# Kernel optimization log

Measured on AMD Instinct MI355X. Metric: run time of the kernel, lower is better.

Reference implementation:

```python
import jax, jax.numpy as jnp
import numpy as np

B, N, DIM = 4, 4096, 512
H, DH = 8, 64
F = 256          # nb_features = min(256, int(log(4096)*32)) = 256
CS = 128         # chunk_size = min(128, n)


def setup_inputs() -> dict:
    key = jax.random.key(0)
    k1, k2, k3, k4 = jax.random.split(key, 4)
    x = jax.random.normal(k1, (B, N, DIM), jnp.float32)
    # scale linear weights like default init so activations stay well-conditioned
    w_qkv = jax.random.normal(k2, (3 * H * DH, DIM), jnp.float32) / jnp.sqrt(DIM)
    w_out = jax.random.normal(k3, (DIM, H * DH), jnp.float32) / jnp.sqrt(H * DH)
    b_out = jnp.zeros((DIM,), jnp.float32)
    # torch.qr(randn(F, DH)) -> reduced Q of shape (F, DH), orthonormal columns
    proj = jnp.linalg.qr(jax.random.normal(k4, (F, DH), jnp.float32))[0]
    return {"x": x, "w_qkv": w_qkv, "w_out": w_out, "b_out": b_out, "proj": proj}


def _kernel_fn(t, proj):
    # exp(x @ proj^T - rowmax), stabilized over the feature axis (as in source)
    tp = jnp.einsum('...d,fd->...f', t, proj)
    return jnp.exp(tp - jnp.max(tp, axis=-1, keepdims=True))


def reference(x, w_qkv, w_out, b_out, proj):
    b, n, _ = x.shape
    scale = DH ** -0.5
    c = n // CS  # number of independent local chunks

    qkv = x @ w_qkv.T                                   # [b, n, 3*h*d]
    q, k, v = jnp.split(qkv, 3, axis=-1)

    def to_chunks(t):  # [b, n, h*d] -> [b, h, c, cs, d]
        return t.reshape(b, n, H, DH).transpose(0, 2, 1, 3).reshape(b, H, c, CS, DH)

    q = to_chunks(q) * scale
    k = to_chunks(k)
    v = to_chunks(v)

    q_prime = _kernel_fn(q, proj)                       # [b, h, c, cs, f]
    k_prime = _kernel_fn(k, proj)                       # [b, h, c, cs, f]

    k_sum = k_prime.sum(axis=3)                         # [b, h, c, f]
    D = jnp.einsum('bhcsf,bhcf->bhcs', q_prime, k_sum)
    D_inv = 1.0 / (D + 0.0001)

    context = jnp.einsum('bhcsf,bhcsd->bhcfd', k_prime, v)     # [b, h, c, f, d]
    out = jnp.einsum('bhcsf,bhcfd->bhcsd', q_prime, context)   # [b, h, c, cs, d]
    out = out * D_inv[..., None]

    out = out.reshape(b, H, n, DH).transpose(0, 2, 1, 3).reshape(b, n, H * DH)
    return out @ w_out.T + b_out                        # dropout p=0 -> identity
```

## Files before the change

kernel.cpp:

```cpp
#include <hip/hip_runtime.h>

#define B_ 4
#define N_ 4096
#define DIM_ 512
#define H_ 8
#define DH_ 64
#define F_ 256
#define CS_ 128
#define M_ (B_*N_)
#define NCHUNK_ 1024

typedef __attribute__((ext_vector_type(8))) short bf16x8;
typedef __attribute__((ext_vector_type(4))) float f32x4;

__device__ __forceinline__ unsigned short f2bf(float x){
  unsigned int u = __float_as_uint(x);
  u += 0x7fffu + ((u >> 16) & 1u);
  return (unsigned short)(u >> 16);
}
__device__ __forceinline__ float bf2f(unsigned short s){
  return __uint_as_float(((unsigned int)s) << 16);
}
__device__ __forceinline__ unsigned pack2(float a, float b){
  return (unsigned)f2bf(a) | ((unsigned)f2bf(b) << 16);
}
__device__ __forceinline__ void gl2lds16(const unsigned short* g, unsigned short* l) {
  __builtin_amdgcn_global_load_lds((const __attribute__((address_space(1))) unsigned int*)g,
                                   (__attribute__((address_space(3))) unsigned int*)l,
                                   16, 0, 0);
}

__global__ __launch_bounds__(256)
void split_kernel(const float* __restrict__ src, unsigned short* __restrict__ hi,
                  unsigned short* __restrict__ lo, int n4)
{
  int idx = blockIdx.x * 256 + threadIdx.x;
  if (idx >= n4) return;
  float4 v = ((const float4*)src)[idx];
  unsigned short h0 = f2bf(v.x), h1 = f2bf(v.y), h2 = f2bf(v.z), h3 = f2bf(v.w);
  unsigned short e0 = f2bf(v.x - bf2f(h0)), e1 = f2bf(v.y - bf2f(h1));
  unsigned short e2 = f2bf(v.z - bf2f(h2)), e3 = f2bf(v.w - bf2f(h3));
  uint2 hv, lv;
  hv.x = (unsigned)h0 | ((unsigned)h1 << 16); hv.y = (unsigned)h2 | ((unsigned)h3 << 16);
  lv.x = (unsigned)e0 | ((unsigned)e1 << 16); lv.y = (unsigned)e2 | ((unsigned)e3 << 16);
  ((uint2*)hi)[idx] = hv;
  ((uint2*)lo)[idx] = lv;
}

__global__ __launch_bounds__(256)
void prep_proj(const float* __restrict__ proj, unsigned short* __restrict__ pq,
               unsigned short* __restrict__ pk)
{
  int idx = blockIdx.x * 256 + threadIdx.x;
  if (idx >= 4096) return;
  float4 v = ((const float4*)proj)[idx];
  uint2 k, q;
  k.x = pack2(v.x, v.y);           k.y = pack2(v.z, v.w);
  q.x = pack2(v.x*0.125f, v.y*0.125f); q.y = pack2(v.z*0.125f, v.w*0.125f);
  ((uint2*)pk)[idx] = k;
  ((uint2*)pq)[idx] = q;
}

template<int SPLIT, int OUT>
__global__ __launch_bounds__(256, 2)
void mfma_gemm_nt(const unsigned short* __restrict__ Ahi, const unsigned short* __restrict__ Alo,
                  const unsigned short* __restrict__ Bhi, const unsigned short* __restrict__ Blo,
                  void* __restrict__ Cm, const float* __restrict__ bias, int K, int ldc,
                  unsigned short* __restrict__ vth, unsigned short* __restrict__ vtl)
{
  __shared__ __align__(16) unsigned short sAhi[4096];
  __shared__ __align__(16) unsigned short sBhi[4096];
  __shared__ __align__(16) unsigned short sAlo[4096];
  __shared__ __align__(16) unsigned short sBlo[4096];
  const int tid = threadIdx.x, lane = tid & 63, wave = tid >> 6;
  const int bm = blockIdx.y * 128, bn = blockIdx.x * 128;
  const int srow0 = wave * 32 + (lane >> 2);
  const int srow1 = srow0 + 16;
  const int slot = lane & 3;
  const int g0 = slot ^ ((srow0 >> 1) & 3);
  const int g1 = slot ^ ((srow1 >> 1) & 3);
  const size_t aOff0 = (size_t)(bm + srow0) * K + g0 * 8;
  const size_t aOff1 = (size_t)(bm + srow1) * K + g1 * 8;
  const size_t bOff0 = (size_t)(bn + srow0) * K + g0 * 8;
  const size_t bOff1 = (size_t)(bn + srow1) * K + g1 * 8;
  const int l0 = wave * 1024, l1 = wave * 1024 + 512;
  const int fr = lane & 15, quad = lane >> 4;
  const int wr = (wave >> 1) * 64, wc = (wave & 1) * 64;
  int offA[4], offB[4];
#pragma unroll
  for (int i = 0; i < 4; ++i) {
    int ra = wr + i * 16 + fr;  offA[i] = ra * 32 + (quad ^ ((ra >> 1) & 3)) * 8;
    int rb = wc + i * 16 + fr;  offB[i] = rb * 32 + (quad ^ ((rb >> 1) & 3)) * 8;
  }
  f32x4 acc[4][4];
#pragma unroll
  for (int i = 0; i < 4; ++i)
#pragma unroll
    for (int j = 0; j < 4; ++j) acc[i][j] = {0.f, 0.f, 0.f, 0.f};

  for (int k0 = 0; k0 < K; k0 += 32) {
    gl2lds16(Ahi + aOff0 + k0, &sAhi[l0]);
    gl2lds16(Ahi + aOff1 + k0, &sAhi[l1]);
    gl2lds16(Bhi + bOff0 + k0, &sBhi[l0]);
    gl2lds16(Bhi + bOff1 + k0, &sBhi[l1]);
    if (SPLIT) {
      gl2lds16(Alo + aOff0 + k0, &sAlo[l0]);
      gl2lds16(Alo + aOff1 + k0, &sAlo[l1]);
      gl2lds16(Blo + bOff0 + k0, &sBlo[l0]);
      gl2lds16(Blo + bOff1 + k0, &sBlo[l1]);
    }
    __syncthreads();
    bf16x8 ah[4], bh[4], al[4], bl[4];
#pragma unroll
    for (int i = 0; i < 4; ++i) {
      ah[i] = *(const bf16x8*)&sAhi[offA[i]];
      bh[i] = *(const bf16x8*)&sBhi[offB[i]];
      if (SPLIT) {
        al[i] = *(const bf16x8*)&sAlo[offA[i]];
        bl[i] = *(const bf16x8*)&sBlo[offB[i]];
      }
    }
#pragma unroll
    for (int i = 0; i < 4; ++i)
#pragma unroll
      for (int j = 0; j < 4; ++j) {
        acc[i][j] = __builtin_amdgcn_mfma_f32_16x16x32_bf16(ah[i], bh[j], acc[i][j], 0, 0, 0);
        if (SPLIT) {
          acc[i][j] = __builtin_amdgcn_mfma_f32_16x16x32_bf16(ah[i], bl[j], acc[i][j], 0, 0, 0);
          acc[i][j] = __builtin_amdgcn_mfma_f32_16x16x32_bf16(al[i], bh[j], acc[i][j], 0, 0, 0);
        }
      }
    __syncthreads();
  }
#pragma unroll
  for (int j = 0; j < 4; ++j) {
    int col = bn + wc + j * 16 + fr;
    float bv = (OUT == 0 && bias) ? bias[col] : 0.f;
#pragma unroll
    for (int i = 0; i < 4; ++i) {
      int row0 = bm + wr + i * 16 + quad * 4;
      if (OUT == 0) {
        float* cp = (float*)Cm + (size_t)row0 * ldc + col;
#pragma unroll
        for (int r = 0; r < 4; ++r) cp[(size_t)r * ldc] = acc[i][j][r] + bv;
      } else if (OUT == 1) {
        unsigned short* cp = (unsigned short*)Cm + (size_t)row0 * ldc + col;
#pragma unroll
        for (int r = 0; r < 4; ++r) cp[(size_t)r * ldc] = f2bf(acc[i][j][r]);
      } else {
        int hh = col >> 6, d = col & 63;
        int bb = row0 >> 12, cc2 = (row0 >> 7) & 31, s = row0 & 127;
        int ck = bb * 256 + hh * 32 + cc2;
        size_t ad = (size_t)ck * 8192 + d * 128 + (((s >> 3) ^ (d & 15)) << 3) + (s & 7);
        float v0 = acc[i][j][0], v1 = acc[i][j][1], v2 = acc[i][j][2], v3 = acc[i][j][3];
        unsigned short h0 = f2bf(v0), h1 = f2bf(v1), h2 = f2bf(v2), h3 = f2bf(v3);
        uint2 hv, lv;
        hv.x = (unsigned)h0 | ((unsigned)h1 << 16);
        hv.y = (unsigned)h2 | ((unsigned)h3 << 16);
        lv.x = pack2(v0 - bf2f(h0), v1 - bf2f(h1));
        lv.y = pack2(v2 - bf2f(h2), v3 - bf2f(h3));
        *(uint2*)(vth + ad) = hv;
        *(uint2*)(vtl + ad) = lv;
      }
    }
  }
}

__global__ __launch_bounds__(256, 2)
void feat_kernel(const unsigned short* __restrict__ qkv_bf,
                 const unsigned short* __restrict__ projq,
                 const unsigned short* __restrict__ projk,
                 unsigned short* __restrict__ qp_g, unsigned short* __restrict__ kpT_g,
                 float* __restrict__ ksum_g)
{
  __shared__ __align__(16) unsigned short IN[8192];
  __shared__ __align__(16) unsigned short BOUNCE[16384];
  __shared__ float KSP[4][256];
  const int tid = threadIdx.x, lane = tid & 63, wave = tid >> 6;
  const int fr = lane & 15, quad = lane >> 4;
  const int chunk = blockIdx.x, p = blockIdx.y;
  const int b = chunk >> 8, h = (chunk >> 5) & 7, cc = chunk & 31;
  const int mbase = b * N_ + cc * CS_;
  const int colbase = p * DIM_ + h * DH_;

#pragma unroll
  for (int j = 0; j < 8; ++j) {
    int idx = tid + j * 256;
    int s = idx >> 4, d0 = (idx & 15) * 4;
    uint2 v = *(const uint2*)(qkv_bf + (size_t)(mbase + s) * 1024 + colbase + d0);
    *(uint2*)(IN + s * 64 + (((d0 >> 3) ^ (s & 7)) << 3) + (d0 & 7)) = v;
  }
  __syncthreads();

  if (p == 0) {
    f32x4 acc[16][2];
#pragma unroll
    for (int mt = 0; mt < 16; ++mt) { acc[mt][0] = {0,0,0,0}; acc[mt][1] = {0,0,0,0}; }
#pragma unroll
    for (int ks = 0; ks < 2; ++ks) {
      bf16x8 bfr[2];
#pragma unroll
      for (int nt = 0; nt < 2; ++nt) {
        int s = wave * 32 + nt * 16 + fr;
        bfr[nt] = *(const bf16x8*)(IN + s * 64 + (((ks * 4 + quad) ^ (s & 7)) << 3));
      }
#pragma unroll
      for (int mt = 0; mt < 16; ++mt) {
        bf16x8 af = *(const bf16x8*)(projq + (size_t)(mt * 16 + fr) * 64 + ks * 32 + quad * 8);
        acc[mt][0] = __builtin_amdgcn_mfma_f32_16x16x32_bf16(af, bfr[0], acc[mt][0], 0, 0, 0);
        acc[mt][1] = __builtin_amdgcn_mfma_f32_16x16x32_bf16(af, bfr[1], acc[mt][1], 0, 0, 0);
      }
    }
#pragma unroll
    for (int nt = 0; nt < 2; ++nt) {
      float m = -1e30f;
#pragma unroll
      for (int mt = 0; mt < 16; ++mt)
#pragma unroll
        for (int r = 0; r < 4; ++r) m = fmaxf(m, acc[mt][nt][r]);
      m = fmaxf(m, __shfl_xor(m, 16, 64));
      m = fmaxf(m, __shfl_xor(m, 32, 64));
#pragma unroll
      for (int mt = 0; mt < 16; ++mt)
#pragma unroll
        for (int r = 0; r < 4; ++r) acc[mt][nt][r] = __expf(acc[mt][nt][r] - m);
    }
    unsigned short* dst = qp_g + (size_t)chunk * 32768;
#pragma unroll
    for (int hf = 0; hf < 2; ++hf) {
      if ((wave >> 1) == hf) {
#pragma unroll
        for (int nt = 0; nt < 2; ++nt) {
          int sl = (wave & 1) * 32 + nt * 16 + fr;
#pragma unroll
          for (int mt = 0; mt < 16; ++mt) {
            int g = mt * 2 + (quad >> 1);
            uint2 w;
            w.x = pack2(acc[mt][nt][0], acc[mt][nt][1]);
            w.y = pack2(acc[mt][nt][2], acc[mt][nt][3]);
            *(uint2*)(BOUNCE + sl * 256 + ((g ^ fr) << 3) + (quad & 1) * 4) = w;
          }
        }
      }
      __syncthreads();
#pragma unroll
      for (int j2 = 0; j2 < 8; ++j2) {
        int idx = j2 * 256 + tid;
        *(float4*)(dst + (size_t)hf * 16384 + idx * 8) = *(const float4*)(BOUNCE + idx * 8);
      }
      __syncthreads();
    }
  } else {
    f32x4 acc[2][16];
#pragma unroll
    for (int nt = 0; nt < 16; ++nt) { acc[0][nt] = {0,0,0,0}; acc[1][nt] = {0,0,0,0}; }
#pragma unroll
    for (int ks = 0; ks < 2; ++ks) {
      bf16x8 a[2];
#pragma unroll
      for (int mt = 0; mt < 2; ++mt) {
        int s = wave * 32 + mt * 16 + fr;
        a[mt] = *(const bf16x8*)(IN + s * 64 + (((ks * 4 + quad) ^ (s & 7)) << 3));
      }
#pragma unroll
      for (int nt = 0; nt < 16; ++nt) {
        bf16x8 bf = *(const bf16x8*)(projk + (size_t)(nt * 16 + fr) * 64 + ks * 32 + quad * 8);
        acc[0][nt] = __builtin_amdgcn_mfma_f32_16x16x32_bf16(a[0], bf, acc[0][nt], 0, 0, 0);
        acc[1][nt] = __builtin_amdgcn_mfma_f32_16x16x32_bf16(a[1], bf, acc[1][nt], 0, 0, 0);
      }
    }
#pragma unroll
    for (int mt = 0; mt < 2; ++mt)
#pragma unroll
      for (int r = 0; r < 4; ++r) {
        float m = acc[mt][0][r];
#pragma unroll
        for (int nt = 1; nt < 16; ++nt) m = fmaxf(m, acc[mt][nt][r]);
        m = fmaxf(m, __shfl_xor(m, 1, 16));
        m = fmaxf(m, __shfl_xor(m, 2, 16));
        m = fmaxf(m, __shfl_xor(m, 4, 16));
        m = fmaxf(m, __shfl_xor(m, 8, 16));
#pragma unroll
        for (int nt = 0; nt < 16; ++nt) acc[mt][nt][r] = __expf(acc[mt][nt][r] - m);
      }
#pragma unroll
    for (int nt = 0; nt < 16; ++nt) {
      float sm = 0.f;
#pragma unroll
      for (int mt = 0; mt < 2; ++mt)
#pragma unroll
        for (int r = 0; r < 4; ++r) sm += acc[mt][nt][r];
      sm += __shfl_xor(sm, 16, 64);
      sm += __shfl_xor(sm, 32, 64);
      if (quad == 0) KSP[wave][nt * 16 + fr] = sm;
    }
    unsigned short* dst = kpT_g + (size_t)chunk * 32768;
#pragma unroll
    for (int hf = 0; hf < 2; ++hf) {
#pragma unroll
      for (int nt2 = 0; nt2 < 8; ++nt2) {
        int nt = hf * 8 + nt2;
        int frow = (nt2 * 16 + fr);
#pragma unroll
        for (int mt = 0; mt < 2; ++mt) {
          int g = wave * 4 + mt * 2 + (quad >> 1);
          uint2 w;
          w.x = pack2(acc[mt][nt][0], acc[mt][nt][1]);
          w.y = pack2(acc[mt][nt][2], acc[mt][nt][3]);
          *(uint2*)(BOUNCE + frow * 128 + ((g ^ fr) << 3) + (quad & 1) * 4) = w;
        }
      }
      __syncthreads();
#pragma unroll
      for (int j2 = 0; j2 < 8; ++j2) {
        int idx = j2 * 256 + tid;
        *(float4*)(dst + (size_t)hf * 16384 + idx * 8) = *(const float4*)(BOUNCE + idx * 8);
      }
      __syncthreads();
    }
    ksum_g[(size_t)chunk * 256 + tid] = KSP[0][tid] + KSP[1][tid] + KSP[2][tid] + KSP[3][tid];
  }
}

__global__ __launch_bounds__(256, 1)
void chunk_kernel(const unsigned short* __restrict__ kpT_g, const unsigned short* __restrict__ qp_g,
                  const unsigned short* __restrict__ vth_g, const unsigned short* __restrict__ vtl_g,
                  const float* __restrict__ ksum_g,
                  unsigned short* __restrict__ attn_hi, unsigned short* __restrict__ attn_lo)
{
  __shared__ __align__(16) char smem[163840];
  unsigned short* LDS = (unsigned short*)smem;
  float* KS = (float*)(smem + 65536);
  float* DI = (float*)(smem + 66560);
  const int tid = threadIdx.x, lane = tid & 63, wave = tid >> 6;
  const int fr = lane & 15, quad = lane >> 4;
  const int chunk = blockIdx.x;
  const int b = chunk >> 8, h = (chunk >> 5) & 7, cc = chunk & 31;
  const int lofs = lane * 8;
  const unsigned short* kps = kpT_g + (size_t)chunk * 32768;
  const unsigned short* qps = qp_g + (size_t)chunk * 32768;
  const unsigned short* vhs = vth_g + (size_t)chunk * 8192;
  const unsigned short* vls = vtl_g + (size_t)chunk * 8192;
#pragma unroll
  for (int i = 0; i < 16; ++i) gl2lds16(kps + (wave*16+i)*512 + lofs, LDS + (wave*16+i)*512);
#pragma unroll
  for (int i = 0; i < 4; ++i)  gl2lds16(vhs + (wave*4+i)*512 + lofs, LDS + 32768 + (wave*4+i)*512);
#pragma unroll
  for (int i = 0; i < 4; ++i)  gl2lds16(vls + (wave*4+i)*512 + lofs, LDS + 40960 + (wave*4+i)*512);
  __syncthreads();
#pragma unroll
  for (int i = 0; i < 16; ++i) gl2lds16(qps + (wave*16+i)*512 + lofs, LDS + 49152 + (wave*16+i)*512);

  f32x4 acc[4][4];
#pragma unroll
  for (int i = 0; i < 4; ++i)
#pragma unroll
    for (int j = 0; j < 4; ++j) acc[i][j] = {0.f, 0.f, 0.f, 0.f};
#pragma unroll
  for (int ks = 0; ks < 4; ++ks) {
    int l = ks * 4 + quad;
    bf16x8 a[4];
#pragma unroll
    for (int mt = 0; mt < 4; ++mt) {
      int f = wave * 64 + mt * 16 + fr;
      a[mt] = *(const bf16x8*)(LDS + f * 128 + ((l ^ (f & 15)) << 3));
    }
#pragma unroll
    for (int nt = 0; nt < 4; ++nt) {
      int d = nt * 16 + fr;
      bf16x8 bh = *(const bf16x8*)(LDS + 32768 + d * 128 + ((l ^ (d & 15)) << 3));
      bf16x8 bl = *(const bf16x8*)(LDS + 40960 + d * 128 + ((l ^ (d & 15)) << 3));
#pragma unroll
      for (int mt = 0; mt < 4; ++mt) {
        acc[mt][nt] = __builtin_amdgcn_mfma_f32_16x16x32_bf16(a[mt], bh, acc[mt][nt], 0, 0, 0);
        acc[mt][nt] = __builtin_amdgcn_mfma_f32_16x16x32_bf16(a[mt], bl, acc[mt][nt], 0, 0, 0);
      }
    }
  }
  __syncthreads();
  KS[tid] = ksum_g[(size_t)chunk * 256 + tid];
#pragma unroll
  for (int mt = 0; mt < 4; ++mt)
#pragma unroll
    for (int nt = 0; nt < 4; ++nt)
#pragma unroll
      for (int r = 0; r < 4; ++r) {
        int f = wave * 64 + mt * 16 + quad * 4 + r;
        int d = nt * 16 + fr;
        float v = acc[mt][nt][r];
        unsigned short hi = f2bf(v);
        unsigned short lo = f2bf(v - bf2f(hi));
        int ad = d * 256 + (((f >> 3) ^ (d & 15)) << 3) + (f & 7);
        LDS[ad] = hi; LDS[16384 + ad] = lo;
      }
  __syncthreads();
  if (tid < 128) {
    int s = tid;
    float dp = 0.f;
#pragma unroll 4
    for (int l = 0; l < 32; ++l) {
      bf16x8 qv = *(const bf16x8*)(LDS + 49152 + s * 256 + ((l ^ (s & 15)) << 3));
      f32x4 k0 = *(const f32x4*)(KS + l * 8);
      f32x4 k1 = *(const f32x4*)(KS + l * 8 + 4);
      dp += bf2f((unsigned short)qv[0]) * k0[0];
      dp += bf2f((unsigned short)qv[1]) * k0[1];
      dp += bf2f((unsigned short)qv[2]) * k0[2];
      dp += bf2f((unsigned short)qv[3]) * k0[3];
      dp += bf2f((unsigned short)qv[4]) * k1[0];
      dp += bf2f((unsigned short)qv[5]) * k1[1];
      dp += bf2f((unsigned short)qv[6]) * k1[2];
      dp += bf2f((unsigned short)qv[7]) * k1[3];
    }
    DI[s] = 1.f / (dp + 1e-4f);
  }
  __syncthreads();
  f32x4 acc2[2][4];
#pragma unroll
  for (int i = 0; i < 2; ++i)
#pragma unroll
    for (int j = 0; j < 4; ++j) acc2[i][j] = {0.f, 0.f, 0.f, 0.f};
#pragma unroll
  for (int ks = 0; ks < 8; ++ks) {
    int l = ks * 4 + quad;
    bf16x8 a[2];
#pragma unroll
    for (int mt = 0; mt < 2; ++mt) {
      int s = wave * 32 + mt * 16 + fr;
      a[mt] = *(const bf16x8*)(LDS + 49152 + s * 256 + ((l ^ (s & 15)) << 3));
    }
#pragma unroll
    for (int nt = 0; nt < 4; ++nt) {
      int d = nt * 16 + fr;
      bf16x8 bh = *(const bf16x8*)(LDS + d * 256 + ((l ^ (d & 15)) << 3));
      bf16x8 bl = *(const bf16x8*)(LDS + 16384 + d * 256 + ((l ^ (d & 15)) << 3));
#pragma unroll
      for (int mt = 0; mt < 2; ++mt) {
        acc2[mt][nt] = __builtin_amdgcn_mfma_f32_16x16x32_bf16(a[mt], bh, acc2[mt][nt], 0, 0, 0);
        acc2[mt][nt] = __builtin_amdgcn_mfma_f32_16x16x32_bf16(a[mt], bl, acc2[mt][nt], 0, 0, 0);
      }
    }
  }
#pragma unroll
  for (int mt = 0; mt < 2; ++mt)
#pragma unroll
    for (int nt = 0; nt < 4; ++nt)
#pragma unroll
      for (int r = 0; r < 4; ++r) {
        int s = wave * 32 + mt * 16 + quad * 4 + r;
        int d = nt * 16 + fr;
        float v = acc2[mt][nt][r] * DI[s];
        unsigned short hi = f2bf(v);
        unsigned short lo = f2bf(v - bf2f(hi));
        size_t off = (size_t)(b * N_ + cc * CS_ + s) * 512 + h * DH_ + d;
        attn_hi[off] = hi; attn_lo[off] = lo;
      }
}

extern "C" void kernel_launch(void* const* d_in, const int* in_sizes, int n_in,
                              void* d_out, int out_size, void* d_ws, size_t ws_size,
                              hipStream_t stream)
{
  const float* x     = (const float*)d_in[0];
  const float* w_qkv = (const float*)d_in[1];
  const float* w_out = (const float*)d_in[2];
  const float* b_out = (const float*)d_in[3];
  const float* proj  = (const float*)d_in[4];
  float* out = (float*)d_out;

  char* ws = (char*)d_ws;
  unsigned short* qkv_bf = (unsigned short*)ws;
  unsigned short* x_hi   = (unsigned short*)(ws + 33554432);
  unsigned short* x_lo   = x_hi + (size_t)M_ * DIM_;
  unsigned short* qp_g   = (unsigned short*)(ws + 67108864);
  unsigned short* kpT_g  = (unsigned short*)(ws + 134217728);
  unsigned short* vth_g  = (unsigned short*)(ws + 201326592);
  unsigned short* vtl_g  = (unsigned short*)(ws + 218103808);
  float*          ksum_g = (float*)(ws + 234881024);

  unsigned short* wqkv_hi = qp_g;
  unsigned short* wqkv_lo = wqkv_hi + (size_t)(3*DIM_) * DIM_;

  unsigned short* projq = x_hi;
  unsigned short* projk = projq + 16384;
  unsigned short* wout_hi = projk + 16384;
  unsigned short* wout_lo = wout_hi + (size_t)DIM_ * DIM_;

  unsigned short* attn_hi = qkv_bf;
  unsigned short* attn_lo = attn_hi + (size_t)M_ * DIM_;

  split_kernel<<<dim3(M_*DIM_/4/256), 256, 0, stream>>>(x, x_hi, x_lo, M_*DIM_/4);
  split_kernel<<<dim3(3*DIM_*DIM_/4/256), 256, 0, stream>>>(w_qkv, wqkv_hi, wqkv_lo, 3*DIM_*DIM_/4);
  mfma_gemm_nt<0,1><<<dim3(8, M_/128), 256, 0, stream>>>(
      x_hi, x_hi, wqkv_hi, wqkv_hi, qkv_bf, nullptr, DIM_, 1024, nullptr, nullptr);
  mfma_gemm_nt<1,2><<<dim3(4, M_/128), 256, 0, stream>>>(
      x_hi, x_lo, wqkv_hi + (size_t)1024*DIM_, wqkv_lo + (size_t)1024*DIM_,
      nullptr, nullptr, DIM_, 0, vth_g, vtl_g);
  prep_proj<<<dim3(16), 256, 0, stream>>>(proj, projq, projk);
  feat_kernel<<<dim3(NCHUNK_, 2), 256, 0, stream>>>(qkv_bf, projq, projk,
                                                    qp_g, kpT_g, ksum_g);
  chunk_kernel<<<dim3(NCHUNK_), 256, 0, stream>>>(kpT_g, qp_g, vth_g, vtl_g, ksum_g,
                                                  attn_hi, attn_lo);
  split_kernel<<<dim3(DIM_*DIM_/4/256), 256, 0, stream>>>(w_out, wout_hi, wout_lo, DIM_*DIM_/4);
  mfma_gemm_nt<1,0><<<dim3(4, M_/128), 256, 0, stream>>>(
      attn_hi, attn_lo, wout_hi, wout_lo, out, b_out, DIM_, DIM_, nullptr, nullptr);
}
```

Baseline: 300.2 us.

## Fuse feature-map kernel into chunk attention kernel, keep q'/k' in LDS

```diff
diff --git a/kernel.cpp b/kernel.cpp
--- a/kernel.cpp
+++ b/kernel.cpp
@@ -166,122 +166,70 @@
   }
 }
 
-__global__ __launch_bounds__(256, 2)
-void feat_kernel(const unsigned short* __restrict__ qkv_bf,
+__global__ __launch_bounds__(256, 1)
+void fused_chunk(const unsigned short* __restrict__ qkv_bf,
                  const unsigned short* __restrict__ projq,
                  const unsigned short* __restrict__ projk,
-                 unsigned short* __restrict__ qp_g, unsigned short* __restrict__ kpT_g,
-                 float* __restrict__ ksum_g)
+                 const unsigned short* __restrict__ vth_g,
+                 const unsigned short* __restrict__ vtl_g,
+                 unsigned short* __restrict__ attn_hi,
+                 unsigned short* __restrict__ attn_lo)
 {
-  __shared__ __align__(16) unsigned short IN[8192];
-  __shared__ __align__(16) unsigned short BOUNCE[16384];
-  __shared__ float KSP[4][256];
+  __shared__ __align__(16) char smem[153088];
+  unsigned short* KPT = (unsigned short*)smem;
+  unsigned short* QP  = (unsigned short*)(smem + 65536);
+  unsigned short* X   = (unsigned short*)(smem + 131072);
+  float* KS  = (float*)(smem + 147456);
+  float* DI  = (float*)(smem + 148480);
+  float* KSP = (float*)(smem + 148992);
+
   const int tid = threadIdx.x, lane = tid & 63, wave = tid >> 6;
   const int fr = lane & 15, quad = lane >> 4;
-  const int chunk = blockIdx.x, p = blockIdx.y;
+  const int chunk = blockIdx.x;
   const int b = chunk >> 8, h = (chunk >> 5) & 7, cc = chunk & 31;
   const int mbase = b * N_ + cc * CS_;
-  const int colbase = p * DIM_ + h * DH_;
 
 #pragma unroll
   for (int j = 0; j < 8; ++j) {
     int idx = tid + j * 256;
     int s = idx >> 4, d0 = (idx & 15) * 4;
-    uint2 v = *(const uint2*)(qkv_bf + (size_t)(mbase + s) * 1024 + colbase + d0);
-    *(uint2*)(IN + s * 64 + (((d0 >> 3) ^ (s & 7)) << 3) + (d0 & 7)) = v;
-  }
-  __syncthreads();
-
-  if (p == 0) {
-    f32x4 acc[16][2];
-#pragma unroll
-    for (int mt = 0; mt < 16; ++mt) { acc[mt][0] = {0,0,0,0}; acc[mt][1] = {0,0,0,0}; }
-#pragma unroll
-    for (int ks = 0; ks < 2; ++ks) {
-      bf16x8 bfr[2];
-#pragma unroll
-      for (int nt = 0; nt < 2; ++nt) {
-        int s = wave * 32 + nt * 16 + fr;
-        bfr[nt] = *(const bf16x8*)(IN + s * 64 + (((ks * 4 + quad) ^ (s & 7)) << 3));
-      }
-#pragma unroll
-      for (int mt = 0; mt < 16; ++mt) {
-        bf16x8 af = *(const bf16x8*)(projq + (size_t)(mt * 16 + fr) * 64 + ks * 32 + quad * 8);
-        acc[mt][0] = __builtin_amdgcn_mfma_f32_16x16x32_bf16(af, bfr[0], acc[mt][0], 0, 0, 0);
-        acc[mt][1] = __builtin_amdgcn_mfma_f32_16x16x32_bf16(af, bfr[1], acc[mt][1], 0, 0, 0);
-      }
-    }
-#pragma unroll
-    for (int nt = 0; nt < 2; ++nt) {
-      float m = -1e30f;
-#pragma unroll
-      for (int mt = 0; mt < 16; ++mt)
-#pragma unroll
-        for (int r = 0; r < 4; ++r) m = fmaxf(m, acc[mt][nt][r]);
-      m = fmaxf(m, __shfl_xor(m, 16, 64));
-      m = fmaxf(m, __shfl_xor(m, 32, 64));
-#pragma unroll
-      for (int mt = 0; mt < 16; ++mt)
-#pragma unroll
-        for (int r = 0; r < 4; ++r) acc[mt][nt][r] = __expf(acc[mt][nt][r] - m);
-    }
-    unsigned short* dst = qp_g + (size_t)chunk * 32768;
-#pragma unroll
-    for (int hf = 0; hf < 2; ++hf) {
-      if ((wave >> 1) == hf) {
-#pragma unroll
-        for (int nt = 0; nt < 2; ++nt) {
-          int sl = (wave & 1) * 32 + nt * 16 + fr;
-#pragma unroll
-          for (int mt = 0; mt < 16; ++mt) {
-            int g = mt * 2 + (quad >> 1);
-            uint2 w;
-            w.x = pack2(acc[mt][nt][0], acc[mt][nt][1]);
-            w.y = pack2(acc[mt][nt][2], acc[mt][nt][3]);
-            *(uint2*)(BOUNCE + sl * 256 + ((g ^ fr) << 3) + (quad & 1) * 4) = w;
-          }
-        }
-      }
-      __syncthreads();
-#pragma unroll
-      for (int j2 = 0; j2 < 8; ++j2) {
-        int idx = j2 * 256 + tid;
-        *(float4*)(dst + (size_t)hf * 16384 + idx * 8) = *(const float4*)(BOUNCE + idx * 8);
-      }
-      __syncthreads();
-    }
-  } else {
-    f32x4 acc[2][16];
-#pragma unroll
-    for (int nt = 0; nt < 16; ++nt) { acc[0][nt] = {0,0,0,0}; acc[1][nt] = {0,0,0,0}; }
+    uint2 v = *(const uint2*)(qkv_bf + (size_t)(mbase + s) * 1024 + 512 + h * DH_ + d0);
+    *(uint2*)(X + s * 64 + (((d0 >> 3) ^ (s & 7)) << 3) + (d0 & 7)) = v;
+  }
+  __syncthreads();
+
+  {
+    f32x4 ka[2][16];
+#pragma unroll
+    for (int nt = 0; nt < 16; ++nt) { ka[0][nt] = {0,0,0,0}; ka[1][nt] = {0,0,0,0}; }
 #pragma unroll
     for (int ks = 0; ks < 2; ++ks) {
       bf16x8 a[2];
 #pragma unroll
       for (int mt = 0; mt < 2; ++mt) {
         int s = wave * 32 + mt * 16 + fr;
-        a[mt] = *(const bf16x8*)(IN + s * 64 + (((ks * 4 + quad) ^ (s & 7)) << 3));
+        a[mt] = *(const bf16x8*)(X + s * 64 + (((ks * 4 + quad) ^ (s & 7)) << 3));
       }
 #pragma unroll
       for (int nt = 0; nt < 16; ++nt) {
         bf16x8 bf = *(const bf16x8*)(projk + (size_t)(nt * 16 + fr) * 64 + ks * 32 + quad * 8);
-        acc[0][nt] = __builtin_amdgcn_mfma_f32_16x16x32_bf16(a[0], bf, acc[0][nt], 0, 0, 0);
-        acc[1][nt] = __builtin_amdgcn_mfma_f32_16x16x32_bf16(a[1], bf, acc[1][nt], 0, 0, 0);
+        ka[0][nt] = __builtin_amdgcn_mfma_f32_16x16x32_bf16(a[0], bf, ka[0][nt], 0, 0, 0);
+        ka[1][nt] = __builtin_amdgcn_mfma_f32_16x16x32_bf16(a[1], bf, ka[1][nt], 0, 0, 0);
       }
     }
 #pragma unroll
     for (int mt = 0; mt < 2; ++mt)
 #pragma unroll
       for (int r = 0; r < 4; ++r) {
-        float m = acc[mt][0][r];
-#pragma unroll
-        for (int nt = 1; nt < 16; ++nt) m = fmaxf(m, acc[mt][nt][r]);
+        float m = ka[mt][0][r];
+#pragma unroll
+        for (int nt = 1; nt < 16; ++nt) m = fmaxf(m, ka[mt][nt][r]);
         m = fmaxf(m, __shfl_xor(m, 1, 16));
         m = fmaxf(m, __shfl_xor(m, 2, 16));
         m = fmaxf(m, __shfl_xor(m, 4, 16));
         m = fmaxf(m, __shfl_xor(m, 8, 16));
 #pragma unroll
-        for (int nt = 0; nt < 16; ++nt) acc[mt][nt][r] = __expf(acc[mt][nt][r] - m);
+        for (int nt = 0; nt < 16; ++nt) ka[mt][nt][r] = __expf(ka[mt][nt][r] - m);
       }
 #pragma unroll
     for (int nt = 0; nt < 16; ++nt) {
@@ -289,73 +237,95 @@
 #pragma unroll
       for (int mt = 0; mt < 2; ++mt)
 #pragma unroll
-        for (int r = 0; r < 4; ++r) sm += acc[mt][nt][r];
+        for (int r = 0; r < 4; ++r) sm += ka[mt][nt][r];
       sm += __shfl_xor(sm, 16, 64);
       sm += __shfl_xor(sm, 32, 64);
-      if (quad == 0) KSP[wave][nt * 16 + fr] = sm;
-    }
-    unsigned short* dst = kpT_g + (size_t)chunk * 32768;
-#pragma unroll
-    for (int hf = 0; hf < 2; ++hf) {
-#pragma unroll
-      for (int nt2 = 0; nt2 < 8; ++nt2) {
-        int nt = hf * 8 + nt2;
-        int frow = (nt2 * 16 + fr);
-#pragma unroll
-        for (int mt = 0; mt < 2; ++mt) {
-          int g = wave * 4 + mt * 2 + (quad >> 1);
-          uint2 w;
-          w.x = pack2(acc[mt][nt][0], acc[mt][nt][1]);
-          w.y = pack2(acc[mt][nt][2], acc[mt][nt][3]);
-          *(uint2*)(BOUNCE + frow * 128 + ((g ^ fr) << 3) + (quad & 1) * 4) = w;
-        }
-      }
-      __syncthreads();
-#pragma unroll
-      for (int j2 = 0; j2 < 8; ++j2) {
-        int idx = j2 * 256 + tid;
-        *(float4*)(dst + (size_t)hf * 16384 + idx * 8) = *(const float4*)(BOUNCE + idx * 8);
-      }
-      __syncthreads();
-    }
-    ksum_g[(size_t)chunk * 256 + tid] = KSP[0][tid] + KSP[1][tid] + KSP[2][tid] + KSP[3][tid];
-  }
-}
-
-__global__ __launch_bounds__(256, 1)
-void chunk_kernel(const unsigned short* __restrict__ kpT_g, const unsigned short* __restrict__ qp_g,
-                  const unsigned short* __restrict__ vth_g, const unsigned short* __restrict__ vtl_g,
-                  const float* __restrict__ ksum_g,
-                  unsigned short* __restrict__ attn_hi, unsigned short* __restrict__ attn_lo)
-{
-  __shared__ __align__(16) char smem[163840];
-  unsigned short* LDS = (unsigned short*)smem;
-  float* KS = (float*)(smem + 65536);
-  float* DI = (float*)(smem + 66560);
-  const int tid = threadIdx.x, lane = tid & 63, wave = tid >> 6;
-  const int fr = lane & 15, quad = lane >> 4;
-  const int chunk = blockIdx.x;
-  const int b = chunk >> 8, h = (chunk >> 5) & 7, cc = chunk & 31;
-  const int lofs = lane * 8;
-  const unsigned short* kps = kpT_g + (size_t)chunk * 32768;
-  const unsigned short* qps = qp_g + (size_t)chunk * 32768;
+      if (quad == 0) KSP[wave * 256 + nt * 16 + fr] = sm;
+    }
+#pragma unroll
+    for (int nt = 0; nt < 16; ++nt) {
+      int f = nt * 16 + fr;
+#pragma unroll
+      for (int mt = 0; mt < 2; ++mt) {
+        int g = wave * 4 + mt * 2 + (quad >> 1);
+        uint2 w;
+        w.x = pack2(ka[mt][nt][0], ka[mt][nt][1]);
+        w.y = pack2(ka[mt][nt][2], ka[mt][nt][3]);
+        *(uint2*)(KPT + f * 128 + ((g ^ (f & 15)) << 3) + (quad & 1) * 4) = w;
+      }
+    }
+  }
+  __syncthreads();
+
+  KS[tid] = KSP[tid] + KSP[256 + tid] + KSP[512 + tid] + KSP[768 + tid];
+#pragma unroll
+  for (int j = 0; j < 8; ++j) {
+    int idx = tid + j * 256;
+    int s = idx >> 4, d0 = (idx & 15) * 4;
+    uint2 v = *(const uint2*)(qkv_bf + (size_t)(mbase + s) * 1024 + h * DH_ + d0);
+    *(uint2*)(X + s * 64 + (((d0 >> 3) ^ (s & 7)) << 3) + (d0 & 7)) = v;
+  }
+  __syncthreads();
+
+  {
+    f32x4 qa[16][2];
+#pragma unroll
+    for (int mt = 0; mt < 16; ++mt) { qa[mt][0] = {0,0,0,0}; qa[mt][1] = {0,0,0,0}; }
+#pragma unroll
+    for (int ks = 0; ks < 2; ++ks) {
+      bf16x8 bfr[2];
+#pragma unroll
+      for (int nt = 0; nt < 2; ++nt) {
+        int s = wave * 32 + nt * 16 + fr;
+        bfr[nt] = *(const bf16x8*)(X + s * 64 + (((ks * 4 + quad) ^ (s & 7)) << 3));
+      }
+#pragma unroll
+      for (int mt = 0; mt < 16; ++mt) {
+        bf16x8 af = *(const bf16x8*)(projq + (size_t)(mt * 16 + fr) * 64 + ks * 32 + quad * 8);
+        qa[mt][0] = __builtin_amdgcn_mfma_f32_16x16x32_bf16(af, bfr[0], qa[mt][0], 0, 0, 0);
+        qa[mt][1] = __builtin_amdgcn_mfma_f32_16x16x32_bf16(af, bfr[1], qa[mt][1], 0, 0, 0);
+      }
+    }
+#pragma unroll
+    for (int nt = 0; nt < 2; ++nt) {
+      float m = -1e30f;
+#pragma unroll
+      for (int mt = 0; mt < 16; ++mt)
+#pragma unroll
+        for (int r = 0; r < 4; ++r) m = fmaxf(m, qa[mt][nt][r]);
+      m = fmaxf(m, __shfl_xor(m, 16, 64));
+      m = fmaxf(m, __shfl_xor(m, 32, 64));
+#pragma unroll
+      for (int mt = 0; mt < 16; ++mt)
+#pragma unroll
+        for (int r = 0; r < 4; ++r) qa[mt][nt][r] = __expf(qa[mt][nt][r] - m);
+    }
+#pragma unroll
+    for (int nt = 0; nt < 2; ++nt) {
+      int s = wave * 32 + nt * 16 + fr;
+#pragma unroll
+      for (int mt = 0; mt < 16; ++mt) {
+        int g = mt * 2 + (quad >> 1);
+        uint2 w;
+        w.x = pack2(qa[mt][nt][0], qa[mt][nt][1]);
+        w.y = pack2(qa[mt][nt][2], qa[mt][nt][3]);
+        *(uint2*)(QP + s * 256 + ((g ^ (s & 15)) << 3) + (quad & 1) * 4) = w;
+      }
+    }
+  }
+  __syncthreads();
+
   const unsigned short* vhs = vth_g + (size_t)chunk * 8192;
   const unsigned short* vls = vtl_g + (size_t)chunk * 8192;
 #pragma unroll
-  for (int i = 0; i < 16; ++i) gl2lds16(kps + (wave*16+i)*512 + lofs, LDS + (wave*16+i)*512);
-#pragma unroll
-  for (int i = 0; i < 4; ++i)  gl2lds16(vhs + (wave*4+i)*512 + lofs, LDS + 32768 + (wave*4+i)*512);
-#pragma unroll
-  for (int i = 0; i < 4; ++i)  gl2lds16(vls + (wave*4+i)*512 + lofs, LDS + 40960 + (wave*4+i)*512);
-  __syncthreads();
-#pragma unroll
-  for (int i = 0; i < 16; ++i) gl2lds16(qps + (wave*16+i)*512 + lofs, LDS + 49152 + (wave*16+i)*512);
-
-  f32x4 acc[4][4];
+  for (int i = 0; i < 4; ++i) gl2lds16(vhs + (wave*4+i)*512 + lane*8, X + (wave*4+i)*512);
+  __syncthreads();
+
+  f32x4 acc_a[4][4];
 #pragma unroll
   for (int i = 0; i < 4; ++i)
 #pragma unroll
-    for (int j = 0; j < 4; ++j) acc[i][j] = {0.f, 0.f, 0.f, 0.f};
+    for (int j = 0; j < 4; ++j) acc_a[i][j] = {0.f, 0.f, 0.f, 0.f};
 #pragma unroll
   for (int ks = 0; ks < 4; ++ks) {
     int l = ks * 4 + quad;
@@ -363,43 +333,69 @@
 #pragma unroll
     for (int mt = 0; mt < 4; ++mt) {
       int f = wave * 64 + mt * 16 + fr;
-      a[mt] = *(const bf16x8*)(LDS + f * 128 + ((l ^ (f & 15)) << 3));
+      a[mt] = *(const bf16x8*)(KPT + f * 128 + ((l ^ (f & 15)) << 3));
     }
 #pragma unroll
     for (int nt = 0; nt < 4; ++nt) {
       int d = nt * 16 + fr;
-      bf16x8 bh = *(const bf16x8*)(LDS + 32768 + d * 128 + ((l ^ (d & 15)) << 3));
-      bf16x8 bl = *(const bf16x8*)(LDS + 40960 + d * 128 + ((l ^ (d & 15)) << 3));
-#pragma unroll
-      for (int mt = 0; mt < 4; ++mt) {
-        acc[mt][nt] = __builtin_amdgcn_mfma_f32_16x16x32_bf16(a[mt], bh, acc[mt][nt], 0, 0, 0);
-        acc[mt][nt] = __builtin_amdgcn_mfma_f32_16x16x32_bf16(a[mt], bl, acc[mt][nt], 0, 0, 0);
-      }
-    }
-  }
-  __syncthreads();
-  KS[tid] = ksum_g[(size_t)chunk * 256 + tid];
+      bf16x8 bh = *(const bf16x8*)(X + d * 128 + ((l ^ (d & 15)) << 3));
+#pragma unroll
+      for (int mt = 0; mt < 4; ++mt)
+        acc_a[mt][nt] = __builtin_amdgcn_mfma_f32_16x16x32_bf16(a[mt], bh, acc_a[mt][nt], 0, 0, 0);
+    }
+  }
+  __syncthreads();
+#pragma unroll
+  for (int i = 0; i < 4; ++i) gl2lds16(vls + (wave*4+i)*512 + lane*8, X + (wave*4+i)*512);
+  __syncthreads();
+#pragma unroll
+  for (int ks = 0; ks < 4; ++ks) {
+    int l = ks * 4 + quad;
+    bf16x8 a[4];
+#pragma unroll
+    for (int mt = 0; mt < 4; ++mt) {
+      int f = wave * 64 + mt * 16 + fr;
+      a[mt] = *(const bf16x8*)(KPT + f * 128 + ((l ^ (f & 15)) << 3));
+    }
+#pragma unroll
+    for (int nt = 0; nt < 4; ++nt) {
+      int d = nt * 16 + fr;
+      bf16x8 bl = *(const bf16x8*)(X + d * 128 + ((l ^ (d & 15)) << 3));
+#pragma unroll
+      for (int mt = 0; mt < 4; ++mt)
+        acc_a[mt][nt] = __builtin_amdgcn_mfma_f32_16x16x32_bf16(a[mt], bl, acc_a[mt][nt], 0, 0, 0);
+    }
+  }
+  __syncthreads();
+
 #pragma unroll
   for (int mt = 0; mt < 4; ++mt)
 #pragma unroll
-    for (int nt = 0; nt < 4; ++nt)
-#pragma unroll
-      for (int r = 0; r < 4; ++r) {
-        int f = wave * 64 + mt * 16 + quad * 4 + r;
-        int d = nt * 16 + fr;
-        float v = acc[mt][nt][r];
-        unsigned short hi = f2bf(v);
-        unsigned short lo = f2bf(v - bf2f(hi));
-        int ad = d * 256 + (((f >> 3) ^ (d & 15)) << 3) + (f & 7);
-        LDS[ad] = hi; LDS[16384 + ad] = lo;
-      }
-  __syncthreads();
+    for (int nt = 0; nt < 4; ++nt) {
+      int f0 = wave * 64 + mt * 16 + quad * 4;
+      int d = nt * 16 + fr;
+      int g = wave * 8 + mt * 2 + (quad >> 1);
+      float v0 = acc_a[mt][nt][0], v1 = acc_a[mt][nt][1];
+      float v2 = acc_a[mt][nt][2], v3 = acc_a[mt][nt][3];
+      unsigned short h0 = f2bf(v0), h1 = f2bf(v1), h2 = f2bf(v2), h3 = f2bf(v3);
+      uint2 whi, wlo;
+      whi.x = (unsigned)h0 | ((unsigned)h1 << 16);
+      whi.y = (unsigned)h2 | ((unsigned)h3 << 16);
+      wlo.x = pack2(v0 - bf2f(h0), v1 - bf2f(h1));
+      wlo.y = pack2(v2 - bf2f(h2), v3 - bf2f(h3));
+      int ad = d * 256 + ((g ^ (d & 15)) << 3) + (quad & 1) * 4;
+      *(uint2*)(KPT + ad) = whi;
+      *(uint2*)(KPT + 16384 + ad) = wlo;
+      (void)f0;
+    }
+  __syncthreads();
+
   if (tid < 128) {
     int s = tid;
     float dp = 0.f;
 #pragma unroll 4
     for (int l = 0; l < 32; ++l) {
-      bf16x8 qv = *(const bf16x8*)(LDS + 49152 + s * 256 + ((l ^ (s & 15)) << 3));
+      bf16x8 qv = *(const bf16x8*)(QP + s * 256 + ((l ^ (s & 15)) << 3));
       f32x4 k0 = *(const f32x4*)(KS + l * 8);
       f32x4 k1 = *(const f32x4*)(KS + l * 8 + 4);
       dp += bf2f((unsigned short)qv[0]) * k0[0];
@@ -414,46 +410,52 @@
     DI[s] = 1.f / (dp + 1e-4f);
   }
   __syncthreads();
-  f32x4 acc2[2][4];
-#pragma unroll
-  for (int i = 0; i < 2; ++i)
-#pragma unroll
-    for (int j = 0; j < 4; ++j) acc2[i][j] = {0.f, 0.f, 0.f, 0.f};
+
+  f32x4 acc2[4][2];
+#pragma unroll
+  for (int i = 0; i < 4; ++i) { acc2[i][0] = {0,0,0,0}; acc2[i][1] = {0,0,0,0}; }
 #pragma unroll
   for (int ks = 0; ks < 8; ++ks) {
     int l = ks * 4 + quad;
-    bf16x8 a[2];
-#pragma unroll
-    for (int mt = 0; mt < 2; ++mt) {
-      int s = wave * 32 + mt * 16 + fr;
-      a[mt] = *(const bf16x8*)(LDS + 49152 + s * 256 + ((l ^ (s & 15)) << 3));
-    }
-#pragma unroll
-    for (int nt = 0; nt < 4; ++nt) {
-      int d = nt * 16 + fr;
-      bf16x8 bh = *(const bf16x8*)(LDS + d * 256 + ((l ^ (d & 15)) << 3));
-      bf16x8 bl = *(const bf16x8*)(LDS + 16384 + d * 256 + ((l ^ (d & 15)) << 3));
-#pragma unroll
-      for (int mt = 0; mt < 2; ++mt) {
-        acc2[mt][nt] = __builtin_amdgcn_mfma_f32_16x16x32_bf16(a[mt], bh, acc2[mt][nt], 0, 0, 0);
-        acc2[mt][nt] = __builtin_amdgcn_mfma_f32_16x16x32_bf16(a[mt], bl, acc2[mt][nt], 0, 0, 0);
-      }
-    }
-  }
-#pragma unroll
-  for (int mt = 0; mt < 2; ++mt)
-#pragma unroll
-    for (int nt = 0; nt < 4; ++nt)
-#pragma unroll
-      for (int r = 0; r < 4; ++r) {
-        int s = wave * 32 + mt * 16 + quad * 4 + r;
-        int d = nt * 16 + fr;
-        float v = acc2[mt][nt][r] * DI[s];
-        unsigned short hi = f2bf(v);
-        unsigned short lo = f2bf(v - bf2f(hi));
-        size_t off = (size_t)(b * N_ + cc * CS_ + s) * 512 + h * DH_ + d;
-        attn_hi[off] = hi; attn_lo[off] = lo;
-      }
+    bf16x8 ah[4], al[4];
+#pragma unroll
+    for (int mt = 0; mt < 4; ++mt) {
+      int d = mt * 16 + fr;
+      int ad = d * 256 + ((l ^ (d & 15)) << 3);
+      ah[mt] = *(const bf16x8*)(KPT + ad);
+      al[mt] = *(const bf16x8*)(KPT + 16384 + ad);
+    }
+#pragma unroll
+    for (int nt = 0; nt < 2; ++nt) {
+      int s = wave * 32 + nt * 16 + fr;
+      bf16x8 bq = *(const bf16x8*)(QP + s * 256 + ((l ^ (s & 15)) << 3));
+#pragma unroll
+      for (int mt = 0; mt < 4; ++mt) {
+        acc2[mt][nt] = __builtin_amdgcn_mfma_f32_16x16x32_bf16(ah[mt], bq, acc2[mt][nt], 0, 0, 0);
+        acc2[mt][nt] = __builtin_amdgcn_mfma_f32_16x16x32_bf16(al[mt], bq, acc2[mt][nt], 0, 0, 0);
+      }
+    }
+  }
+#pragma unroll
+  for (int nt = 0; nt < 2; ++nt) {
+    int s = wave * 32 + nt * 16 + fr;
+    float di = DI[s];
+    size_t base = (size_t)(mbase + s) * 512 + h * DH_;
+#pragma unroll
+    for (int mt = 0; mt < 4; ++mt) {
+      int d0 = mt * 16 + quad * 4;
+      float o0 = acc2[mt][nt][0] * di, o1 = acc2[mt][nt][1] * di;
+      float o2 = acc2[mt][nt][2] * di, o3 = acc2[mt][nt][3] * di;
+      unsigned short h0 = f2bf(o0), h1 = f2bf(o1), h2 = f2bf(o2), h3 = f2bf(o3);
+      uint2 whi, wlo;
+      whi.x = (unsigned)h0 | ((unsigned)h1 << 16);
+      whi.y = (unsigned)h2 | ((unsigned)h3 << 16);
+      wlo.x = pack2(o0 - bf2f(h0), o1 - bf2f(h1));
+      wlo.y = pack2(o2 - bf2f(h2), o3 - bf2f(h3));
+      *(uint2*)(attn_hi + base + d0) = whi;
+      *(uint2*)(attn_lo + base + d0) = wlo;
+    }
+  }
 }
 
 extern "C" void kernel_launch(void* const* d_in, const int* in_sizes, int n_in,
@@ -471,22 +473,17 @@
   unsigned short* qkv_bf = (unsigned short*)ws;
   unsigned short* x_hi   = (unsigned short*)(ws + 33554432);
   unsigned short* x_lo   = x_hi + (size_t)M_ * DIM_;
-  unsigned short* qp_g   = (unsigned short*)(ws + 67108864);
-  unsigned short* kpT_g  = (unsigned short*)(ws + 134217728);
+  unsigned short* wqkv_hi = (unsigned short*)(ws + 67108864);
+  unsigned short* wqkv_lo = wqkv_hi + (size_t)(3*DIM_) * DIM_;
+  unsigned short* attn_hi = (unsigned short*)(ws + 134217728);
+  unsigned short* attn_lo = attn_hi + (size_t)M_ * DIM_;
   unsigned short* vth_g  = (unsigned short*)(ws + 201326592);
   unsigned short* vtl_g  = (unsigned short*)(ws + 218103808);
-  float*          ksum_g = (float*)(ws + 234881024);
-
-  unsigned short* wqkv_hi = qp_g;
-  unsigned short* wqkv_lo = wqkv_hi + (size_t)(3*DIM_) * DIM_;
 
   unsigned short* projq = x_hi;
   unsigned short* projk = projq + 16384;
   unsigned short* wout_hi = projk + 16384;
   unsigned short* wout_lo = wout_hi + (size_t)DIM_ * DIM_;
-
-  unsigned short* attn_hi = qkv_bf;
-  unsigned short* attn_lo = attn_hi + (size_t)M_ * DIM_;
 
   split_kernel<<<dim3(M_*DIM_/4/256), 256, 0, stream>>>(x, x_hi, x_lo, M_*DIM_/4);
   split_kernel<<<dim3(3*DIM_*DIM_/4/256), 256, 0, stream>>>(w_qkv, wqkv_hi, wqkv_lo, 3*DIM_*DIM_/4);
@@ -496,10 +493,8 @@
       x_hi, x_lo, wqkv_hi + (size_t)1024*DIM_, wqkv_lo + (size_t)1024*DIM_,
       nullptr, nullptr, DIM_, 0, vth_g, vtl_g);
   prep_proj<<<dim3(16), 256, 0, stream>>>(proj, projq, projk);
-  feat_kernel<<<dim3(NCHUNK_, 2), 256, 0, stream>>>(qkv_bf, projq, projk,
-                                                    qp_g, kpT_g, ksum_g);
-  chunk_kernel<<<dim3(NCHUNK_), 256, 0, stream>>>(kpT_g, qp_g, vth_g, vtl_g, ksum_g,
-                                                  attn_hi, attn_lo);
+  fused_chunk<<<dim3(NCHUNK_), 256, 0, stream>>>(qkv_bf, projq, projk, vth_g, vtl_g,
+                                                 attn_hi, attn_lo);
   split_kernel<<<dim3(DIM_*DIM_/4/256), 256, 0, stream>>>(w_out, wout_hi, wout_lo, DIM_*DIM_/4);
   mfma_gemm_nt<1,0><<<dim3(4, M_/128), 256, 0, stream>>>(
       attn_hi, attn_lo, wout_hi, wout_lo, out, b_out, DIM_, DIM_, nullptr, nullptr);
```

New measurement: 281.7 us. -6.2%, faster.
